# Optimization experiments

Hardware: AMD Instinct MI355X
Metric: run time of the kernel (lower is better)

## Reference

```python
import jax, jax.numpy as jnp
import numpy as np

B, N, D, H = 16, 2048, 256, 256  # batch, sensor points, branch dim, hidden dim


def setup_inputs() -> dict:
    key = jax.random.key(0)
    ks = jax.random.split(key, 12)
    s = 0.02
    return {
        "x": jax.random.normal(ks[0], (B, N), dtype=jnp.float32),
        "grid": jax.random.uniform(ks[1], (N, 1), dtype=jnp.float32),  # cellcenters_nx
        "W1a": jax.random.normal(ks[2], (2, H), dtype=jnp.float32) * s,
        "b1a": jnp.zeros((H,), dtype=jnp.float32),
        "W1b": jax.random.normal(ks[3], (H, D), dtype=jnp.float32) * s,
        "b1b": jnp.zeros((D,), dtype=jnp.float32),
        "Wqkv": jax.random.normal(ks[4], (D, 3 * D), dtype=jnp.float32) * s,
        "W2a": jax.random.normal(ks[5], (D, H), dtype=jnp.float32) * s,
        "b2a": jnp.zeros((H,), dtype=jnp.float32),
        "W2b": jax.random.normal(ks[6], (H, D), dtype=jnp.float32) * s,
        "b2b": jnp.zeros((D,), dtype=jnp.float32),
    }


def reference(x, grid, W1a, b1a, W1b, b1b, Wqkv, W2a, b2a, W2b, b2b):
    b, n = x.shape
    # x.unsqueeze(-1) concat grid -> [B, N, 2]
    g = jnp.broadcast_to(grid[None, :, :], (b, n, 1))
    h = jnp.concatenate([x[..., None], g], axis=-1)
    # littleFNN Linear1: Linear -> GELU(exact) -> Linear
    h = jax.nn.gelu(h @ W1a + b1a, approximate=False) @ W1b + b1b  # [B, N, D]
    # SelfAttention: single fused qkv projection, no bias
    qkv = h @ Wqkv  # [B, N, 3D]
    q, k, v = jnp.split(qkv, 3, axis=-1)
    scale = jnp.asarray(qkv.shape[-1] // 3, h.dtype) ** -0.5
    scores = jnp.einsum("bid,bjd->bij", q, k) * scale  # [B, N, N]
    attn = jax.nn.softmax(scores, axis=-1)
    o = jnp.einsum("bij,bjd->bid", attn, v)  # [B, N, D]
    # littleFNN Linear2
    o = jax.nn.gelu(o @ W2a + b2a, approximate=False) @ W2b + b2b  # [B, N, D]
    return jnp.mean(o, axis=1)  # [B, D]
```

## Files before the change

### kernel.cpp

```cpp
#include <hip/hip_runtime.h>
#include <hip/hip_bf16.h>
#include <cmath>

typedef __attribute__((ext_vector_type(8))) short short8;
typedef __attribute__((ext_vector_type(4))) float f32x4;

#define MFMA16(a, b, c) __builtin_amdgcn_mfma_f32_16x16x32_bf16((a), (b), (c), 0, 0, 0)

static constexpr int BB = 16, NN = 2048, DD = 256, HH = 256;

__device__ inline unsigned short f2bf(float f) {
    union { float f; unsigned int u; } v; v.f = f;
    unsigned int r = v.u + 0x7fffu + ((v.u >> 16) & 1u);
    return (unsigned short)(r >> 16);
}
__device__ inline float bf2f(unsigned short u) {
    union { unsigned int u; float f; } v; v.u = ((unsigned int)u) << 16;
    return v.f;
}
__device__ inline float gelu_exact(float x) {
    return 0.5f * x * (1.0f + erff(x * 0.7071067811865475f));
}
__device__ inline void gload_lds16(const void* g, void* l) {
    __builtin_amdgcn_global_load_lds(
        (const __attribute__((address_space(1))) unsigned int*)g,
        (__attribute__((address_space(3))) unsigned int*)l, 16, 0, 0);
}
__device__ inline void fence_mem() { asm volatile("" ::: "memory"); }
__device__ inline unsigned int cvtpk_bf16(float lo, float hi) {
    unsigned int r;
    asm("v_cvt_pk_bf16_f32 %0, %1, %2" : "=v"(r) : "v"(lo), "v"(hi));
    return r;
}

__global__ __launch_bounds__(256) void transposeT_k(const float* __restrict__ W1b,
                                                    const float* __restrict__ Wqkv,
                                                    const float* __restrict__ W2a,
                                                    unsigned short* __restrict__ W1bT,
                                                    unsigned short* __restrict__ WqkvT,
                                                    unsigned short* __restrict__ W2aT) {
    __shared__ float tl[64][65];
    int bid = blockIdx.x;
    const float* src;
    unsigned short* dst;
    int N, tn, tk;
    if (bid < 16) {
        src = W1b; dst = W1bT; N = 256; tn = bid & 3; tk = bid >> 2;
    } else if (bid < 64) {
        int t2 = bid - 16;
        src = Wqkv; dst = WqkvT; N = 768; tn = t2 % 12; tk = t2 / 12;
    } else {
        int t2 = bid - 64;
        src = W2a; dst = W2aT; N = 256; tn = t2 & 3; tk = t2 >> 2;
    }
    int n0 = tn * 64, k0 = tk * 64;
    int t = threadIdx.x;
#pragma unroll
    for (int j = 0; j < 4; j++) {
        int row = (t >> 4) * 4 + j;
        f32x4 v = *(const f32x4*)(src + (size_t)(k0 + row) * N + n0 + (t & 15) * 4);
#pragma unroll
        for (int e = 0; e < 4; e++) tl[row][(t & 15) * 4 + e] = v[e];
    }
    __syncthreads();
    int n = t >> 2, cb = (t & 3) * 16;
    short8 a, b;
#pragma unroll
    for (int e = 0; e < 8; e++) {
        a[e] = (short)f2bf(tl[cb + e][n]);
        b[e] = (short)f2bf(tl[cb + 8 + e][n]);
    }
    *(short8*)(dst + (size_t)(n0 + n) * 256 + k0 + cb) = a;
    *(short8*)(dst + (size_t)(n0 + n) * 256 + k0 + cb + 8) = b;
}

__global__ __launch_bounds__(512) void ffn_qkv_k(const float* __restrict__ x,
                                                 const float* __restrict__ grd,
                                                 const float* __restrict__ W1a,
                                                 const float* __restrict__ b1a,
                                                 const unsigned short* __restrict__ W1bT,
                                                 const float* __restrict__ b1b,
                                                 const unsigned short* __restrict__ WqkvT,
                                                 unsigned short* __restrict__ qo,
                                                 unsigned short* __restrict__ ko,
                                                 unsigned short* __restrict__ vo) {
    __shared__ __attribute__((aligned(16))) char bstage[2][32768];
    __shared__ unsigned short h_lds[4][16 * 256];
    const int w = threadIdx.x >> 6, lane = threadIdx.x & 63;
    const int c = lane & 15, g = lane >> 4;
    const int qsub = w >> 1, nh = w & 1;
    const int rb = blockIdx.x * 64 + qsub * 16;
    const int bb = (blockIdx.x * 64) >> 11;
    const int rowinb = (rb & (NN - 1)) + c;

    const int p0r = rb + c;
    const float xv = x[p0r];
    const float gv = grd[p0r & (NN - 1)];
    short8 tf[8];
#pragma unroll
    for (int kc = 0; kc < 8; kc++) {
        int j0 = kc * 32 + g * 8;
#pragma unroll
        for (int e = 0; e < 8; e += 4) {
            f32x4 wa = *(const f32x4*)(W1a + j0 + e);
            f32x4 wb = *(const f32x4*)(W1a + 256 + j0 + e);
            f32x4 ba = *(const f32x4*)(b1a + j0 + e);
#pragma unroll
            for (int q = 0; q < 4; q++) {
                float v = xv * wa[q] + gv * wb[q] + ba[q];
                tf[kc][e + q] = (short)f2bf(gelu_exact(v));
            }
        }
    }

    const char* Bb0 = (const char*)W1bT;
    const char* Bb1 = (const char*)WqkvT;
    const char* Bb2 = (const char*)WqkvT + 256 * 512;
    const char* Bb3 = (const char*)WqkvT + 512 * 512;

#define STAGE_B(buf_, Bb_, kcp_) do {                                                    \
        _Pragma("unroll")                                                                \
        for (int i_ = 0; i_ < 4; i_++) {                                                 \
            int d_ = i_ * 8192 + w * 1024 + lane * 16;                                   \
            int row_ = d_ >> 7, sl_ = (d_ >> 4) & 7;                                     \
            gload_lds16(Bb_ + (size_t)row_ * 512 + (kcp_) * 128 +                        \
                            ((sl_ ^ (row_ & 7)) << 4),                                   \
                        &bstage[buf_][0] + d_);                                          \
        }                                                                                \
    } while (0)

    short8 hf[8];
#pragma unroll
    for (int kc = 0; kc < 8; kc++) hf[kc] = tf[kc];

    STAGE_B(0, Bb0, 0);

#pragma unroll
    for (int p = 0; p < 4; p++) {
        f32x4 acc[8];
#pragma unroll
        for (int n = 0; n < 8; n++) acc[n] = (f32x4){0.f, 0.f, 0.f, 0.f};

#pragma unroll
        for (int kcp = 0; kcp < 4; kcp++) {
            const int gi = p * 4 + kcp;
            if (gi + 1 < 16) {
                const int ni = gi + 1;
                const char* nb = (ni >> 2) == 0 ? Bb0 : (ni >> 2) == 1 ? Bb1
                                : (ni >> 2) == 2 ? Bb2 : Bb3;
                STAGE_B(ni & 1, nb, ni & 3);
                asm volatile("s_waitcnt vmcnt(4)" ::: "memory");
            } else {
                asm volatile("s_waitcnt vmcnt(0)" ::: "memory");
            }
            __builtin_amdgcn_s_barrier();
            fence_mem();

            const char* bl = &bstage[gi & 1][0];
#pragma unroll
            for (int sub = 0; sub < 2; sub++) {
                short8 a = (p == 0) ? tf[kcp * 2 + sub] : hf[kcp * 2 + sub];
#pragma unroll
                for (int n = 0; n < 8; n++) {
                    int addr = (nh * 128 + n * 16 + c) * 128 +
                               ((((sub << 2) | g) ^ (c & 7)) << 4);
                    short8 bfr = *(const short8*)(bl + addr);
                    if (p == 3) acc[n] = MFMA16(bfr, a, acc[n]);
                    else        acc[n] = MFMA16(a, bfr, acc[n]);
                }
            }
            fence_mem();
            __builtin_amdgcn_s_barrier();
            fence_mem();
        }

        if (p == 0) {
            unsigned short* hl = &h_lds[qsub][0];
#pragma unroll
            for (int n = 0; n < 8; n++) {
                int col = nh * 128 + n * 16 + c;
                float bv = b1b[col];
#pragma unroll
                for (int r = 0; r < 4; r++) {
                    int row = g * 4 + r;
                    hl[row * 256 + (col ^ ((row & 7) << 3))] = f2bf(acc[n][r] + bv);
                }
            }
            __syncthreads();
#pragma unroll
            for (int kc = 0; kc < 8; kc++) {
                hf[kc] = *(const short8*)(hl + c * 256 + ((kc * 32 + g * 8) ^ ((c & 7) << 3)));
            }
        } else if (p == 1) {
#pragma unroll
            for (int n = 0; n < 8; n++)
#pragma unroll
                for (int r = 0; r < 4; r++)
                    qo[(size_t)(rb + g * 4 + r) * 256 + nh * 128 + n * 16 + c] =
                        f2bf(acc[n][r] * (0.0625f * 1.4426950408889634f));
        } else if (p == 2) {
#pragma unroll
            for (int n = 0; n < 8; n++)
#pragma unroll
                for (int r = 0; r < 4; r++)
                    ko[(size_t)(rb + g * 4 + r) * 256 + nh * 128 + n * 16 + c] =
                        f2bf(acc[n][r]);
        } else {
#pragma unroll
            for (int m = 0; m < 8; m++) {
#pragma unroll
                for (int r = 0; r < 4; r++) {
                    int dcol = nh * 128 + m * 16 + g * 4 + r;
                    vo[((size_t)(bb * 256 + dcol)) * NN + rowinb] = f2bf(acc[m][r]);
                }
            }
        }
    }
#undef STAGE_B
}

__global__ __launch_bounds__(512) void attn_k(const unsigned short* __restrict__ qb,
                                              const unsigned short* __restrict__ kb,
                                              const unsigned short* __restrict__ vTb,
                                              const unsigned short* __restrict__ W2aT,
                                              const float* __restrict__ b2a,
                                              float* __restrict__ bar) {
    __shared__ __attribute__((aligned(16))) char smem[74752];
    char* klds = smem;
    char* vlds = smem + 32768;
    unsigned int* p_lds = (unsigned int*)(smem + 65536);
    float* exm = (float*)(smem + 65536 + 8192);
    float* exl = exm + 128;
    const int tid = threadIdx.x;
    const int w = tid >> 6, lane = tid & 63;
    const int c = lane & 15, g = lane >> 4;
    const int qsub = w & 3, dhalf = w >> 2;
    const int khalf = dhalf;
    const int bid = blockIdx.x;
    const int swz = (bid & 7) * 64 + (bid >> 3);
    const int b = swz >> 5;
    const int qt = swz & 31;
    const int qbase = qt * 64 + qsub * 16;
    constexpr int NT = NN / 64;

    const int sl_sub = lane >> 5;
    const int sl_col = (lane & 31) * 16;
    const int vl_row = lane >> 3;
    const size_t vl_off = (size_t)vl_row * (NN * 2) + (size_t)(((lane & 7) ^ vl_row) << 4);

    const short8* qp = (const short8*)(qb + (size_t)(b * NN + qbase + c) * DD + g * 8);
    short8 qf[8];
#pragma unroll
    for (int kc = 0; kc < 8; kc++) qf[kc] = qp[kc * 4];

    const char* kb_bytes = (const char*)(kb + (size_t)(b * NN) * DD);
    const char* vb_bytes = (const char*)(vTb + (size_t)(b * DD) * NN);
    const int kswz = (c & 7) << 4;
    const int pcs = c & 7;

#define STAGE_K(kt_) do {                                                                \
        const char* gk = kb_bytes + ((size_t)((kt_) * 64 + 8 * w)) * 512;                \
        _Pragma("unroll")                                                                \
        for (int s_ = 0; s_ < 4; s_++) {                                                 \
            int row_lo = 2 * s_ + sl_sub;                                                \
            gload_lds16(gk + (size_t)row_lo * 512 + (sl_col ^ (row_lo << 4)),            \
                        klds + (8 * w + 2 * s_) * 512);                                  \
        }                                                                                \
    } while (0)
#define STAGE_V(kt_) do {                                                                \
        const char* gv = vb_bytes + (size_t)(32 * w) * (NN * 2) + (size_t)(kt_) * 128 + vl_off; \
        _Pragma("unroll")                                                                \
        for (int s_ = 0; s_ < 4; s_++) {                                                 \
            gload_lds16(gv + (size_t)(8 * s_) * (NN * 2),                                \
                        vlds + (32 * w + 8 * s_) * 128);                                 \
        }                                                                                \
    } while (0)

    f32x4 oacc[8];
#pragma unroll
    for (int i = 0; i < 8; i++) oacc[i] = (f32x4){0.f, 0.f, 0.f, 0.f};
    float mrun = -INFINITY;
    float lrun = 0.f;
    unsigned int* plw = p_lds + qsub * 512 + c * 32;

    STAGE_K(0);

    for (int kt = 0; kt < NT; kt++) {
        STAGE_V(kt);
        asm volatile("s_waitcnt vmcnt(4)" ::: "memory");
        __builtin_amdgcn_s_barrier();
        fence_mem();

        const char* klb = klds + (size_t)(khalf * 32) * 512;
        f32x4 s0 = (f32x4){0.f, 0.f, 0.f, 0.f};
        f32x4 s1 = (f32x4){0.f, 0.f, 0.f, 0.f};
        __builtin_amdgcn_s_setprio(1);
#pragma unroll
        for (int kc = 0; kc < 8; kc++) {
            short8 qv = qf[kc];
            int col = (kc * 64 + g * 16) ^ kswz;
            short8 kf0 = *(const short8*)(klb + (size_t)c * 512 + col);
            short8 kf1 = *(const short8*)(klb + (size_t)(c + 16) * 512 + col);
            s0 = MFMA16(kf0, qv, s0);
            s1 = MFMA16(kf1, qv, s1);
        }
        __builtin_amdgcn_s_setprio(0);

        float t0 = fmaxf(fmaxf(s0[0], s0[1]), fmaxf(s0[2], s0[3]));
        float t1 = fmaxf(fmaxf(s1[0], s1[1]), fmaxf(s1[2], s1[3]));
        float tmo = fmaxf(t0, t1);
        tmo = fmaxf(tmo, __shfl_xor(tmo, 16));
        tmo = fmaxf(tmo, __shfl_xor(tmo, 32));
        if (g == 0) exm[w * 16 + c] = tmo;
        fence_mem();
        __builtin_amdgcn_s_barrier();
        fence_mem();
        float tmax = fmaxf(tmo, exm[(w ^ 4) * 16 + c]);

        if (kt + 1 < NT) STAGE_K(kt + 1);

        bool need = tmax > mrun + 8.f;
        if (__any(need)) {
            float mn = fmaxf(mrun, tmax);
            float corr = exp2f(mrun - mn);
#pragma unroll
            for (int r = 0; r < 4; r++) s0[r] = exp2f(s0[r] - mn);
#pragma unroll
            for (int r = 0; r < 4; r++) s1[r] = exp2f(s1[r] - mn);
            lrun = lrun * corr + ((s0[0] + s0[1]) + (s0[2] + s0[3])) +
                   ((s1[0] + s1[1]) + (s1[2] + s1[3]));
            mrun = mn;
#pragma unroll
            for (int r = 0; r < 4; r++) {
                float cr = __shfl(corr, 20 * g + r);
#pragma unroll
                for (int nc = 0; nc < 8; nc++) oacc[nc][r] *= cr;
            }
        } else {
#pragma unroll
            for (int r = 0; r < 4; r++) s0[r] = exp2f(s0[r] - mrun);
#pragma unroll
            for (int r = 0; r < 4; r++) s1[r] = exp2f(s1[r] - mrun);
            lrun += ((s0[0] + s0[1]) + (s0[2] + s0[3])) +
                    ((s1[0] + s1[1]) + (s1[2] + s1[3]));
        }

        {
            int jb0 = khalf * 16 + 2 * g;
            int jb1 = khalf * 16 + 8 + 2 * g;
#pragma unroll
            for (int h = 0; h < 2; h++) {
                int j = jb0 + h;
                plw[(((j >> 2) ^ pcs) << 2) | (j & 3)] = cvtpk_bf16(s0[2 * h], s0[2 * h + 1]);
                j = jb1 + h;
                plw[(((j >> 2) ^ pcs) << 2) | (j & 3)] = cvtpk_bf16(s1[2 * h], s1[2 * h + 1]);
            }
        }
        fence_mem();
        if (kt + 1 < NT) {
            asm volatile("s_waitcnt vmcnt(4)" ::: "memory");
        } else {
            asm volatile("s_waitcnt vmcnt(0)" ::: "memory");
        }
        __builtin_amdgcn_s_barrier();
        fence_mem();

        short8 pf0 = *(const short8*)(plw + ((g ^ pcs) << 2));
        short8 pf1 = *(const short8*)(plw + (((4 + g) ^ pcs) << 2));
        __builtin_amdgcn_s_setprio(1);
#pragma unroll
        for (int nc = 0; nc < 8; nc++) {
            const char* vr = vlds + (size_t)(dhalf * 128 + nc * 16 + c) * 128;
            short8 vf0 = *(const short8*)(vr + ((g ^ pcs) << 4));
            short8 vf1 = *(const short8*)(vr + (((4 + g) ^ pcs) << 4));
            oacc[nc] = MFMA16(pf0, vf0, oacc[nc]);
            oacc[nc] = MFMA16(pf1, vf1, oacc[nc]);
        }
        __builtin_amdgcn_s_setprio(0);

        fence_mem();
        __builtin_amdgcn_s_barrier();
        fence_mem();
    }
#undef STAGE_K
#undef STAGE_V

    float lt = lrun;
    lt += __shfl_xor(lt, 16);
    lt += __shfl_xor(lt, 32);
    if (g == 0) exl[w * 16 + c] = lt;
    fence_mem();
    __builtin_amdgcn_s_barrier();
    fence_mem();
    lt += exl[(w ^ 4) * 16 + c];
    float inv_r[4];
#pragma unroll
    for (int r = 0; r < 4; r++) inv_r[r] = 1.f / __shfl(lt, 20 * g + r);

    unsigned short* ol = (unsigned short*)smem;
#pragma unroll
    for (int r = 0; r < 4; r++) {
        int row = 4 * g + r;
        int swr = (row & 7) << 3;
#pragma unroll
        for (int nc = 0; nc < 8; nc++) {
            int col = dhalf * 128 + nc * 16 + c;
            ol[qsub * 4096 + row * 256 + (col ^ swr)] = f2bf(oacc[nc][r] * inv_r[r]);
        }
    }
    fence_mem();
    __builtin_amdgcn_s_barrier();
    fence_mem();

    {
        const int wcol = w * 32;
        float colsum[2] = {0.f, 0.f};
#pragma unroll
        for (int q2 = 0; q2 < 4; q2++) {
            f32x4 acc2[2];
            acc2[0] = (f32x4){0.f, 0.f, 0.f, 0.f};
            acc2[1] = (f32x4){0.f, 0.f, 0.f, 0.f};
            const unsigned short* oq = ol + q2 * 4096;
            const int swc = (c & 7) << 3;
#pragma unroll
            for (int kc = 0; kc < 8; kc++) {
                short8 a = *(const short8*)(oq + c * 256 + ((kc * 32 + g * 8) ^ swc));
#pragma unroll
                for (int nc = 0; nc < 2; nc++) {
                    short8 bfr = *(const short8*)(W2aT + (size_t)(wcol + nc * 16 + c) * 256 + kc * 32 + g * 8);
                    acc2[nc] = MFMA16(a, bfr, acc2[nc]);
                }
            }
#pragma unroll
            for (int nc = 0; nc < 2; nc++) {
                float bv = b2a[wcol + nc * 16 + c];
                float s2 = 0.f;
#pragma unroll
                for (int r = 0; r < 4; r++) s2 += gelu_exact(acc2[nc][r] + bv);
                colsum[nc] += s2;
            }
        }
#pragma unroll
        for (int nc = 0; nc < 2; nc++) {
            float s2 = colsum[nc];
            s2 += __shfl_xor(s2, 16);
            s2 += __shfl_xor(s2, 32);
            if (g == 0) atomicAdd(&bar[b * 256 + wcol + nc * 16 + c], s2);
        }
    }
}

__global__ void final_k(const float* __restrict__ bar, const float* __restrict__ W2b,
                        const float* __restrict__ b2b, float* __restrict__ out) {
    int b = blockIdx.x, d = threadIdx.x;
    float s = 0.f;
    for (int h = 0; h < HH; h++) s += bar[b * HH + h] * W2b[h * DD + d];
    out[b * DD + d] = b2b[d] + s * (1.f / (float)NN);
}

extern "C" void kernel_launch(void* const* d_in, const int* in_sizes, int n_in,
                              void* d_out, int out_size, void* d_ws, size_t ws_size,
                              hipStream_t stream) {
    (void)in_sizes; (void)n_in; (void)out_size; (void)ws_size;
    const float* x    = (const float*)d_in[0];
    const float* grd  = (const float*)d_in[1];
    const float* W1a  = (const float*)d_in[2];
    const float* b1a  = (const float*)d_in[3];
    const float* W1b  = (const float*)d_in[4];
    const float* b1b  = (const float*)d_in[5];
    const float* Wqkv = (const float*)d_in[6];
    const float* W2a  = (const float*)d_in[7];
    const float* b2a  = (const float*)d_in[8];
    const float* W2b  = (const float*)d_in[9];
    const float* b2b  = (const float*)d_in[10];
    float* out = (float*)d_out;

    char* ws = (char*)d_ws;
    const size_t MB = 1024 * 1024;
    unsigned short* q_buf  = (unsigned short*)(ws + 0);
    unsigned short* k_buf  = (unsigned short*)(ws + 16 * MB);
    unsigned short* vT_buf = (unsigned short*)(ws + 32 * MB);
    unsigned short* W1bT   = (unsigned short*)(ws + 80 * MB);
    unsigned short* WqkvT  = (unsigned short*)(ws + 80 * MB + 512 * 1024);
    unsigned short* W2aT   = (unsigned short*)(ws + 81 * MB);
    float*          bar    = (float*)(ws + 81 * MB + 256 * 1024);

    transposeT_k<<<dim3(80), 256, 0, stream>>>(W1b, Wqkv, W2a, W1bT, WqkvT, W2aT);
    ffn_qkv_k<<<dim3(512), 512, 0, stream>>>(x, grd, W1a, b1a, W1bT, b1b, WqkvT,
                                             q_buf, k_buf, vT_buf);
    hipMemsetAsync(bar, 0, BB * HH * sizeof(float), stream);
    attn_k<<<dim3(512), 512, 0, stream>>>(q_buf, k_buf, vT_buf, W2aT, b2a, bar);
    final_k<<<dim3(BB), 256, 0, stream>>>(bar, W2b, b2b, out);
}
```

Measured before the change: 197.8 us.

## Track per-key-half softmax max separately to drop a mid-tile barrier

```diff
diff --git a/kernel.cpp b/kernel.cpp
--- a/kernel.cpp
+++ b/kernel.cpp
@@ -225,12 +225,14 @@
                                               const unsigned short* __restrict__ W2aT,
                                               const float* __restrict__ b2a,
                                               float* __restrict__ bar) {
-    __shared__ __attribute__((aligned(16))) char smem[74752];
+    __shared__ __attribute__((aligned(16))) char smem[75392];
     char* klds = smem;
     char* vlds = smem + 32768;
     unsigned int* p_lds = (unsigned int*)(smem + 65536);
-    float* exm = (float*)(smem + 65536 + 8192);
-    float* exl = exm + 128;
+    float* crl = (float*)(smem + 73728);
+    int* flg = (int*)(smem + 74240);
+    float* exm = (float*)(smem + 74304);
+    float* exl = (float*)(smem + 74816);
     const int tid = threadIdx.x;
     const int w = tid >> 6, lane = tid & 63;
     const int c = lane & 15, g = lane >> 4;
@@ -276,9 +278,12 @@
         }                                                                                \
     } while (0)
 
-    f32x4 oacc[8];
-#pragma unroll
-    for (int i = 0; i < 8; i++) oacc[i] = (f32x4){0.f, 0.f, 0.f, 0.f};
+    f32x4 oa[8], ob2[8];
+#pragma unroll
+    for (int i = 0; i < 8; i++) {
+        oa[i] = (f32x4){0.f, 0.f, 0.f, 0.f};
+        ob2[i] = (f32x4){0.f, 0.f, 0.f, 0.f};
+    }
     float mrun = -INFINITY;
     float lrun = 0.f;
     unsigned int* plw = p_lds + qsub * 512 + c * 32;
@@ -308,19 +313,13 @@
 
         float t0 = fmaxf(fmaxf(s0[0], s0[1]), fmaxf(s0[2], s0[3]));
         float t1 = fmaxf(fmaxf(s1[0], s1[1]), fmaxf(s1[2], s1[3]));
-        float tmo = fmaxf(t0, t1);
-        tmo = fmaxf(tmo, __shfl_xor(tmo, 16));
-        tmo = fmaxf(tmo, __shfl_xor(tmo, 32));
-        if (g == 0) exm[w * 16 + c] = tmo;
-        fence_mem();
-        __builtin_amdgcn_s_barrier();
-        fence_mem();
-        float tmax = fmaxf(tmo, exm[(w ^ 4) * 16 + c]);
-
-        if (kt + 1 < NT) STAGE_K(kt + 1);
+        float tmax = fmaxf(t0, t1);
+        tmax = fmaxf(tmax, __shfl_xor(tmax, 16));
+        tmax = fmaxf(tmax, __shfl_xor(tmax, 32));
 
         bool need = tmax > mrun + 8.f;
-        if (__any(need)) {
+        int fl = __any(need) ? 1 : 0;
+        if (fl) {
             float mn = fmaxf(mrun, tmax);
             float corr = exp2f(mrun - mn);
 #pragma unroll
@@ -330,12 +329,7 @@
             lrun = lrun * corr + ((s0[0] + s0[1]) + (s0[2] + s0[3])) +
                    ((s1[0] + s1[1]) + (s1[2] + s1[3]));
             mrun = mn;
-#pragma unroll
-            for (int r = 0; r < 4; r++) {
-                float cr = __shfl(corr, 20 * g + r);
-#pragma unroll
-                for (int nc = 0; nc < 8; nc++) oacc[nc][r] *= cr;
-            }
+            if (g == 0) crl[(qsub * 2 + khalf) * 16 + c] = corr;
         } else {
 #pragma unroll
             for (int r = 0; r < 4; r++) s0[r] = exp2f(s0[r] - mrun);
@@ -344,6 +338,7 @@
             lrun += ((s0[0] + s0[1]) + (s0[2] + s0[3])) +
                     ((s1[0] + s1[1]) + (s1[2] + s1[3]));
         }
+        if (lane == 0) flg[qsub * 2 + khalf] = fl;
 
         {
             int jb0 = khalf * 16 + 2 * g;
@@ -357,13 +352,28 @@
             }
         }
         fence_mem();
-        if (kt + 1 < NT) {
-            asm volatile("s_waitcnt vmcnt(4)" ::: "memory");
-        } else {
-            asm volatile("s_waitcnt vmcnt(0)" ::: "memory");
-        }
+        asm volatile("s_waitcnt vmcnt(0)" ::: "memory");
         __builtin_amdgcn_s_barrier();
         fence_mem();
+
+        if (kt + 1 < NT) STAGE_K(kt + 1);
+
+        int f0 = flg[qsub * 2 + 0];
+        int f1 = flg[qsub * 2 + 1];
+        if (f0) {
+            f32x4 ca = *(const f32x4*)(crl + (qsub * 2 + 0) * 16 + 4 * g);
+#pragma unroll
+            for (int nc = 0; nc < 8; nc++)
+#pragma unroll
+                for (int r = 0; r < 4; r++) oa[nc][r] *= ca[r];
+        }
+        if (f1) {
+            f32x4 cb = *(const f32x4*)(crl + (qsub * 2 + 1) * 16 + 4 * g);
+#pragma unroll
+            for (int nc = 0; nc < 8; nc++)
+#pragma unroll
+                for (int r = 0; r < 4; r++) ob2[nc][r] *= cb[r];
+        }
 
         short8 pf0 = *(const short8*)(plw + ((g ^ pcs) << 2));
         short8 pf1 = *(const short8*)(plw + (((4 + g) ^ pcs) << 2));
@@ -373,8 +383,8 @@
             const char* vr = vlds + (size_t)(dhalf * 128 + nc * 16 + c) * 128;
             short8 vf0 = *(const short8*)(vr + ((g ^ pcs) << 4));
             short8 vf1 = *(const short8*)(vr + (((4 + g) ^ pcs) << 4));
-            oacc[nc] = MFMA16(pf0, vf0, oacc[nc]);
-            oacc[nc] = MFMA16(pf1, vf1, oacc[nc]);
+            oa[nc] = MFMA16(pf0, vf0, oa[nc]);
+            ob2[nc] = MFMA16(pf1, vf1, ob2[nc]);
         }
         __builtin_amdgcn_s_setprio(0);
 
@@ -388,14 +398,27 @@
     float lt = lrun;
     lt += __shfl_xor(lt, 16);
     lt += __shfl_xor(lt, 32);
-    if (g == 0) exl[w * 16 + c] = lt;
+    if (g == 0) { exm[w * 16 + c] = mrun; exl[w * 16 + c] = lt; }
     fence_mem();
     __builtin_amdgcn_s_barrier();
     fence_mem();
-    lt += exl[(w ^ 4) * 16 + c];
-    float inv_r[4];
-#pragma unroll
-    for (int r = 0; r < 4; r++) inv_r[r] = 1.f / __shfl(lt, 20 * g + r);
+    float m_oth = exm[(w ^ 4) * 16 + c];
+    float l_oth = exl[(w ^ 4) * 16 + c];
+    float m0 = (khalf == 0) ? mrun : m_oth;
+    float l0 = (khalf == 0) ? lt : l_oth;
+    float m1 = (khalf == 0) ? m_oth : mrun;
+    float l1 = (khalf == 0) ? l_oth : lt;
+    float M = fmaxf(m0, m1);
+    float sa = exp2f(m0 - M);
+    float sb = exp2f(m1 - M);
+    float inv = 1.f / (l0 * sa + l1 * sb);
+    float sar[4], sbr[4], inv_r[4];
+#pragma unroll
+    for (int r = 0; r < 4; r++) {
+        sar[r] = __shfl(sa, 20 * g + r);
+        sbr[r] = __shfl(sb, 20 * g + r);
+        inv_r[r] = __shfl(inv, 20 * g + r);
+    }
 
     unsigned short* ol = (unsigned short*)smem;
 #pragma unroll
@@ -405,7 +428,8 @@
 #pragma unroll
         for (int nc = 0; nc < 8; nc++) {
             int col = dhalf * 128 + nc * 16 + c;
-            ol[qsub * 4096 + row * 256 + (col ^ swr)] = f2bf(oacc[nc][r] * inv_r[r]);
+            float ov = (oa[nc][r] * sar[r] + ob2[nc][r] * sbr[r]) * inv_r[r];
+            ol[qsub * 4096 + row * 256 + (col ^ swr)] = f2bf(ov);
         }
     }
     fence_mem();
```

Measured after the change: 199.3 us. No clear change (+0.8%).
